# Performance work log

Measured on AMD Instinct MI355X. Metric: run time of the kernel, lower is better.

## Reference

```python
import jax, jax.numpy as jnp
import numpy as np
from math import comb

K = 10
N_NODES = 100000
NUM_FEATURES = 512
HIDDEN = 256
NUM_CLASSES = 64
N_EDGES = 3200000


def setup_inputs() -> dict:
    key = jax.random.key(0)
    k = jax.random.split(key, 8)
    x = jax.random.normal(k[0], (N_NODES, NUM_FEATURES), dtype=jnp.float32)
    src = jax.random.randint(k[1], (N_EDGES,), 0, N_NODES, dtype=jnp.int32)
    dst = jax.random.randint(k[2], (N_EDGES,), 0, N_NODES, dtype=jnp.int32)
    # symmetrize so the sym-normalized Laplacian is well-defined (undirected graph)
    src2 = jnp.concatenate([src, dst])
    dst2 = jnp.concatenate([dst, src])
    edge_index = jnp.stack([src2, dst2], axis=0)  # [2, 2E]
    s1 = 1.0 / np.sqrt(NUM_FEATURES)
    s2 = 1.0 / np.sqrt(HIDDEN)
    W1 = jax.random.uniform(k[3], (NUM_FEATURES, HIDDEN), jnp.float32, -s1, s1)
    b1 = jax.random.uniform(k[4], (HIDDEN,), jnp.float32, -s1, s1)
    W2 = jax.random.uniform(k[5], (HIDDEN, NUM_CLASSES), jnp.float32, -s2, s2)
    b2 = jax.random.uniform(k[6], (NUM_CLASSES,), jnp.float32, -s2, s2)
    temp = jnp.ones((K + 1,), dtype=jnp.float32)  # reset_parameters fills with 1
    return {"x": x, "edge_index": edge_index, "W1": W1, "b1": b1, "W2": W2, "b2": b2, "temp": temp}


def bern_prop(h, src, dst, temp, num_nodes):
    # sym-normalized adjacency weights: w = d^{-1/2}[src] * d^{-1/2}[dst]
    deg = jax.ops.segment_sum(jnp.ones_like(src, dtype=h.dtype), src, num_segments=num_nodes)
    dis = jnp.where(deg > 0, jax.lax.rsqrt(jnp.maximum(deg, 1e-30)), 0.0)
    w = dis[src] * dis[dst]  # [E]

    def adj(v):  # A_hat @ v via gather + scatter-add (source_to_target flow)
        return jax.ops.segment_sum(w[:, None] * v[src], dst, num_segments=num_nodes)

    TEMP = jax.nn.relu(temp)
    coef = np.array([comb(K, i) / 2.0 ** K for i in range(K + 1)], dtype=np.float32)

    tmp = [h]
    for _ in range(K):  # (2I - L) h = h + A_hat h
        h = h + adj(h)
        tmp.append(h)
    out = coef[0] * TEMP[0] * tmp[K]
    for i in range(K):
        y = tmp[K - i - 1]
        for _ in range(i + 1):  # L y = y - A_hat y
            y = y - adj(y)
        out = out + coef[i + 1] * TEMP[i + 1] * y
    return out


def reference(x, edge_index, W1, b1, W2, b2, temp):
    # eval mode: dropout is identity
    h = jax.nn.relu(x @ W1 + b1)
    h = h @ W2 + b2  # [N, num_classes]
    src, dst = edge_index[0], edge_index[1]
    h = bern_prop(h, src, dst, temp, x.shape[0])
    return jax.nn.log_softmax(h, axis=1)
```

## Files before the change

kernel.cpp:

```cpp
#include <hip/hip_runtime.h>
#include <hip/hip_bf16.h>
#include <hip/hip_cooperative_groups.h>
#include <math.h>


#define KORD 10

namespace cg = cooperative_groups;

typedef __attribute__((ext_vector_type(8))) short bf16x8;
typedef __attribute__((ext_vector_type(4))) float f32x4;

typedef __attribute__((address_space(1))) const unsigned int* gas_t;
typedef __attribute__((address_space(3))) unsigned int* las_t;

static __device__ __forceinline__ void gll16(const void* g, void* l) {
    __builtin_amdgcn_global_load_lds((gas_t)g, (las_t)l, 16, 0, 0);
}

static __device__ __forceinline__ ushort f2bf(float f) {
    unsigned u = __float_as_uint(f);
    unsigned r = (u + 0x7fffu + ((u >> 16) & 1u)) >> 16;
    return (ushort)r;
}
static __device__ __forceinline__ float bf2f(ushort h) {
    return __uint_as_float(((unsigned)h) << 16);
}
static __device__ __forceinline__ uint pack2(float a, float b) {
    return (uint)f2bf(a) | ((uint)f2bf(b) << 16);
}

__global__ void prep_all(const float* __restrict__ temp,
                         const float* __restrict__ W1, const float* __restrict__ W2,
                         float* __restrict__ acoef, int* __restrict__ flags,
                         ushort* __restrict__ w1b,
                         ushort* __restrict__ w2h, ushort* __restrict__ w2l)
{
    int tid = blockIdx.x * 256 + threadIdx.x;
    if (tid == 0) {
        int C[KORD + 1][KORD + 1];
        for (int n = 0; n <= KORD; ++n) {
            for (int k = 0; k <= KORD; ++k) C[n][k] = 0;
            C[n][0] = 1;
            for (int k = 1; k <= n; ++k)
                C[n][k] = C[n - 1][k - 1] + ((k <= n - 1) ? C[n - 1][k] : 0);
        }
        float a[KORD + 1];
        for (int j = 0; j <= KORD; ++j) a[j] = 0.f;
        for (int m = 0; m <= KORD; ++m) {
            float tm = temp[m];
            tm = tm > 0.f ? tm : 0.f;
            float cm = (float)C[KORD][m] / 1024.0f;
            for (int p = 0; p <= m; ++p)
                for (int q = 0; q <= KORD - m; ++q) {
                    int Mij = ((p & 1) ? -1 : 1) * C[m][p] * C[KORD - m][q];
                    a[p + q] += cm * tm * (float)Mij;
                }
        }
        for (int j = 0; j <= KORD; ++j) acoef[j] = a[j];
        int any = 0;
        for (int j = KORD; j >= 0; --j) {
            if (a[j] != 0.f) any = 1;
            flags[j] = any;
        }
    }
    if (tid < 512 * 256) {
        int j = tid & 7, lg = (tid >> 3) & 3, col = (tid >> 5) & 255, kt = tid >> 13;
        int k = kt * 32 + lg * 8 + j;
        w1b[tid] = f2bf(W1[k * 256 + col]);
    } else if (tid < 512 * 256 + 256 * 64) {
        int t2 = tid - 512 * 256;
        int j = t2 & 7, lg = (t2 >> 3) & 3, col = (t2 >> 5) & 63, ks = t2 >> 11;
        int k = ks * 32 + lg * 8 + j;
        float v = W2[k * 64 + col];
        ushort hi = f2bf(v);
        ushort lo = f2bf(v - bf2f(hi));
        w2h[t2] = hi; w2l[t2] = lo;
    }
}

__global__ __launch_bounds__(512, 4) void mlp_kernel(
    const float* __restrict__ x,
    const ushort* __restrict__ w1b,
    const ushort* __restrict__ w2h, const ushort* __restrict__ w2l,
    const float* __restrict__ b1, const float* __restrict__ b2,
    float* __restrict__ v0, float* __restrict__ out,
    const float* __restrict__ acoef, const int* __restrict__ flags, int N)
{
    __shared__ __align__(16) char sm[65536];

    const int t    = threadIdx.x;
    const int lane = t & 63;
    const int wid  = t >> 6;
    const int wm   = wid >> 2;
    const int wn   = wid & 3;
    const int l15  = lane & 15;
    const int lg   = lane >> 4;
    const int tile = blockIdx.x;
    const int row0 = tile * 128;

    f32x4 acc[4][4];
#pragma unroll
    for (int i = 0; i < 4; ++i)
#pragma unroll
        for (int j = 0; j < 4; ++j) acc[i][j] = (f32x4)0.f;

    const int sr = t >> 2;
    const int sq = t & 3;
    int rl = row0 + sr; if (rl > N - 1) rl = N - 1;
    const float* xsrc = x + (size_t)rl * 512 + sq * 8;
    ushort* xb0 = (ushort*)sm;
    ushort* xb1 = (ushort*)(sm + 8192);
    uint4* xdst0 = (uint4*)(sm + t * 16);
    uint4* xdst1 = (uint4*)(sm + 8192 + t * 16);

    const char* w1base = (const char*)w1b;
    char* bb0 = sm + 16384;
    char* bb1 = sm + 32768;

    float4 xa0 = *(const float4*)(xsrc);
    float4 xa1 = *(const float4*)(xsrc + 4);
#pragma unroll
    for (int i = 0; i < 2; ++i)
        gll16(w1base + (size_t)wid * 2048 + i * 1024 + lane * 16,
              bb0 + wid * 2048 + i * 1024);
    float4 xc0 = *(const float4*)(xsrc + 32);
    float4 xc1 = *(const float4*)(xsrc + 36);
    *xdst0 = make_uint4(pack2(xa0.x, xa0.y), pack2(xa0.z, xa0.w),
                        pack2(xa1.x, xa1.y), pack2(xa1.z, xa1.w));
    __syncthreads();

    for (int kt2 = 0; kt2 < 16; kt2 += 2) {
        {
            int ktn = kt2 + 1;
#pragma unroll
            for (int i = 0; i < 2; ++i)
                gll16(w1base + (size_t)ktn * 16384 + wid * 2048 + i * 1024 + lane * 16,
                      bb1 + wid * 2048 + i * 1024);
            int ktx = kt2 + 2; if (ktx > 15) ktx = 15;
            xa0 = *(const float4*)(xsrc + ktx * 32);
            xa1 = *(const float4*)(xsrc + ktx * 32 + 4);

            bf16x8 Ah[4];
#pragma unroll
            for (int mf = 0; mf < 4; ++mf)
                Ah[mf] = *(const bf16x8*)&xb0[((wm * 4 + mf) * 64 + l15 * 4 + lg) * 8];
#pragma unroll
            for (int nf = 0; nf < 4; ++nf) {
                bf16x8 B = *(const bf16x8*)(bb0 + (wn * 64 + nf * 16 + l15) * 64 + lg * 16);
#pragma unroll
                for (int mf = 0; mf < 4; ++mf)
                    acc[mf][nf] = __builtin_amdgcn_mfma_f32_16x16x32_bf16(Ah[mf], B, acc[mf][nf], 0, 0, 0);
            }
            *xdst1 = make_uint4(pack2(xc0.x, xc0.y), pack2(xc0.z, xc0.w),
                                pack2(xc1.x, xc1.y), pack2(xc1.z, xc1.w));
            __syncthreads();
        }
        {
            int ktn = kt2 + 2; if (ktn > 15) ktn = 15;
#pragma unroll
            for (int i = 0; i < 2; ++i)
                gll16(w1base + (size_t)ktn * 16384 + wid * 2048 + i * 1024 + lane * 16,
                      bb0 + wid * 2048 + i * 1024);
            int ktx = kt2 + 3; if (ktx > 15) ktx = 15;
            xc0 = *(const float4*)(xsrc + ktx * 32);
            xc1 = *(const float4*)(xsrc + ktx * 32 + 4);

            bf16x8 Ah[4];
#pragma unroll
            for (int mf = 0; mf < 4; ++mf)
                Ah[mf] = *(const bf16x8*)&xb1[((wm * 4 + mf) * 64 + l15 * 4 + lg) * 8];
#pragma unroll
            for (int nf = 0; nf < 4; ++nf) {
                bf16x8 B = *(const bf16x8*)(bb1 + (wn * 64 + nf * 16 + l15) * 64 + lg * 16);
#pragma unroll
                for (int mf = 0; mf < 4; ++mf)
                    acc[mf][nf] = __builtin_amdgcn_mfma_f32_16x16x32_bf16(Ah[mf], B, acc[mf][nf], 0, 0, 0);
            }
            *xdst0 = make_uint4(pack2(xa0.x, xa0.y), pack2(xa0.z, xa0.w),
                                pack2(xa1.x, xa1.y), pack2(xa1.z, xa1.w));
            __syncthreads();
        }
    }

    ushort* h1l = (ushort*)sm;
#pragma unroll
    for (int nf = 0; nf < 4; ++nf) {
        int col = wn * 64 + nf * 16 + l15;
        float bb = b1[col];
        int ks = col >> 5, lgw = (col >> 3) & 3, j = col & 7;
#pragma unroll
        for (int mf = 0; mf < 4; ++mf) {
            int g = wm * 4 + mf;
#pragma unroll
            for (int r = 0; r < 4; ++r) {
                float v = acc[mf][nf][r] + bb;
                v = fmaxf(v, 0.f);
                int l15w = lg * 4 + r;
                h1l[(((ks * 8 + g) * 64) + l15w * 4 + lgw) * 8 + j] = f2bf(v);
            }
        }
    }
    __syncthreads();

    f32x4 acc2[4];
#pragma unroll
    for (int i = 0; i < 4; ++i) acc2[i] = (f32x4)0.f;
#pragma unroll
    for (int ks = 0; ks < 8; ++ks) {
        bf16x8 A = *(const bf16x8*)&h1l[((ks * 8 + wid) * 64 + l15 * 4 + lg) * 8];
#pragma unroll
        for (int nf = 0; nf < 4; ++nf) {
            size_t bo = (size_t)ks * 2048 + (nf * 16 + l15) * 32 + (lg << 3);
            bf16x8 Bh = *(const bf16x8*)(w2h + bo);
            bf16x8 Bl = *(const bf16x8*)(w2l + bo);
            acc2[nf] = __builtin_amdgcn_mfma_f32_16x16x32_bf16(A, Bh, acc2[nf], 0, 0, 0);
            acc2[nf] = __builtin_amdgcn_mfma_f32_16x16x32_bf16(A, Bl, acc2[nf], 0, 0, 0);
        }
    }

    int flag1 = flags[0 + 1];
    float a0c = acoef[0];
    float z[4][4];
#pragma unroll
    for (int nf = 0; nf < 4; ++nf) {
        float bb = b2[nf * 16 + l15];
#pragma unroll
        for (int r = 0; r < 4; ++r) z[nf][r] = acc2[nf][r] + bb;
    }
    if (!flag1) {
#pragma unroll
        for (int r = 0; r < 4; ++r) {
            int row = row0 + wid * 16 + lg * 4 + r;
            float mx = fmaxf(fmaxf(z[0][r], z[1][r]), fmaxf(z[2][r], z[3][r]));
#pragma unroll
            for (int off = 1; off < 16; off <<= 1) mx = fmaxf(mx, __shfl_xor(mx, off, 64));
            float s = expf(z[0][r] - mx) + expf(z[1][r] - mx)
                    + expf(z[2][r] - mx) + expf(z[3][r] - mx);
#pragma unroll
            for (int off = 1; off < 16; off <<= 1) s += __shfl_xor(s, off, 64);
            float lns = logf(s);
            if (row < N) {
#pragma unroll
                for (int nf = 0; nf < 4; ++nf)
                    out[(size_t)row * 64 + nf * 16 + l15] = z[nf][r] - mx - lns;
            }
        }
    } else {
#pragma unroll
        for (int nf = 0; nf < 4; ++nf) {
            int col = nf * 16 + l15;
#pragma unroll
            for (int r = 0; r < 4; ++r) {
                int row = row0 + wid * 16 + lg * 4 + r;
                if (row < N) {
                    size_t o = (size_t)row * 64 + col;
                    v0[o] = z[nf][r];
                    out[o] = a0c * z[nf][r];
                }
            }
        }
    }
}

__global__ __launch_bounds__(256) void graph_coop(
    const int* __restrict__ src, const int* __restrict__ dst, int E, int N,
    int* __restrict__ degs, int* __restrict__ degd, int* __restrict__ cursor,
    int* __restrict__ rowp, int* __restrict__ csrs, float* __restrict__ csrw,
    float* __restrict__ v0, float* __restrict__ v1, float* __restrict__ out,
    const float* __restrict__ acoef, const int* __restrict__ flags)
{
    __shared__ int sums[256];
    if (!flags[1]) return;
    cg::grid_group grid = cg::this_grid();
    int gtid = blockIdx.x * 256 + threadIdx.x;
    int gstr = gridDim.x * 256;

    for (int i = gtid; i < N; i += gstr) { degs[i] = 0; degd[i] = 0; cursor[i] = 0; }
    grid.sync();
    for (int e = gtid; e < E; e += gstr) {
        atomicAdd(&degs[src[e]], 1);
        atomicAdd(&degd[dst[e]], 1);
    }
    grid.sync();
    if (blockIdx.x == 0) {
        int tid = threadIdx.x;
        int chunk = (N + 255) / 256;
        int s0 = tid * chunk;
        int s1 = s0 + chunk; if (s1 > N) s1 = N; if (s0 > N) s0 = N;
        int s = 0;
        for (int i = s0; i < s1; ++i) s += degd[i];
        sums[tid] = s;
        __syncthreads();
        for (int off = 1; off < 256; off <<= 1) {
            int v = (tid >= off) ? sums[tid - off] : 0;
            __syncthreads();
            sums[tid] += v;
            __syncthreads();
        }
        int run = sums[tid] - s;
        for (int i = s0; i < s1; ++i) { rowp[i] = run; run += degd[i]; }
        if (tid == 255) rowp[N] = sums[255];
    }
    grid.sync();
    for (int e = gtid; e < E; e += gstr) {
        int s = src[e], d = dst[e];
        int dgs = degs[s], dgd = degs[d];
        float ws_ = (dgs > 0 ? rsqrtf((float)dgs) : 0.f)
                  * (dgd > 0 ? rsqrtf((float)dgd) : 0.f);
        int slot = rowp[d] + atomicAdd(&cursor[d], 1);
        csrs[slot] = s;
        csrw[slot] = ws_;
    }
    grid.sync();
    const float* va = v0;
    float* vb = v1;
    int lane = threadIdx.x & 63;
    int grpbase = lane & 48;
    for (int j = 1; j <= KORD; ++j) {
        if (!flags[j]) break;
        float aj = acoef[j];
        for (int idx = gtid; idx < N * 16; idx += gstr) {
            int n = idx >> 4;
            int q = idx & 15;
            int beg = rowp[n], end = rowp[n + 1];
            float4 acc = make_float4(0.f, 0.f, 0.f, 0.f);
            for (int base = beg; base < end; base += 16) {
                int s = 0; float wvv = 0.f;
                int ii = base + q;
                if (ii < end) { s = csrs[ii]; wvv = csrw[ii]; }
                int m = end - base; if (m > 16) m = 16;
                for (int u = 0; u < m; ++u) {
                    int ss = __shfl(s, grpbase + u, 64);
                    float ww = __shfl(wvv, grpbase + u, 64);
                    float4 vv = *(const float4*)(va + ((long)ss << 6) + (q << 2));
                    acc.x += ww * vv.x; acc.y += ww * vv.y;
                    acc.z += ww * vv.z; acc.w += ww * vv.w;
                }
            }
            long o = ((long)n << 6) + (q << 2);
            *(float4*)(vb + o) = acc;
            float4 ov = *(const float4*)(out + o);
            ov.x += aj * acc.x; ov.y += aj * acc.y;
            ov.z += aj * acc.z; ov.w += aj * acc.w;
            *(float4*)(out + o) = ov;
        }
        grid.sync();
        float* tsw = vb; vb = (float*)va; va = tsw;
    }
    for (int idx = gtid; idx < N * 64; idx += gstr) {
        int n = idx >> 6;
        int c = idx & 63;
        float v = out[(long)n * 64 + c];
        float mx = v;
#pragma unroll
        for (int off = 32; off; off >>= 1) mx = fmaxf(mx, __shfl_xor(mx, off, 64));
        float e = expf(v - mx);
        float s = e;
#pragma unroll
        for (int off = 32; off; off >>= 1) s += __shfl_xor(s, off, 64);
        out[(long)n * 64 + c] = v - mx - logf(s);
    }
}

extern "C" void kernel_launch(void* const* d_in, const int* in_sizes, int n_in,
                              void* d_out, int out_size, void* d_ws, size_t ws_size,
                              hipStream_t stream)
{
    const float* x    = (const float*)d_in[0];
    const int*   ei   = (const int*)d_in[1];
    const float* W1   = (const float*)d_in[2];
    const float* b1   = (const float*)d_in[3];
    const float* W2   = (const float*)d_in[4];
    const float* b2   = (const float*)d_in[5];
    const float* temp = (const float*)d_in[6];

    int N = in_sizes[0] / 512;
    int E = in_sizes[1] / 2;
    const int* src = ei;
    const int* dst = ei + E;
    float* out = (float*)d_out;

    char* w = (char*)d_ws;
    auto alloc = [&](size_t bytes) {
        char* p = w;
        w += (bytes + 255) & ~(size_t)255;
        return p;
    };
    float* acoef  = (float*)alloc(64);
    int*   flags  = (int*)alloc(64);
    int*   degs   = (int*)alloc((size_t)N * 4);
    int*   degd   = (int*)alloc((size_t)N * 4);
    int*   cursor = (int*)alloc((size_t)N * 4);
    int*   rowp   = (int*)alloc((size_t)(N + 1) * 4);
    int*   csrs   = (int*)alloc((size_t)E * 4);
    float* csrw   = (float*)alloc((size_t)E * 4);
    ushort* w1b   = (ushort*)alloc(512 * 256 * 2);
    ushort* w2h   = (ushort*)alloc(256 * 64 * 2);
    ushort* w2l   = (ushort*)alloc(256 * 64 * 2);
    float* v0     = (float*)alloc((size_t)N * 64 * 4);
    float* v1     = (float*)alloc((size_t)N * 64 * 4);

    prep_all<<<576, 256, 0, stream>>>(temp, W1, W2, acoef, flags, w1b, w2h, w2l);

    int ntiles = (N + 127) / 128;
    mlp_kernel<<<ntiles, 512, 0, stream>>>(x, w1b, w2h, w2l, b1, b2, v0, out,
                                           acoef, flags, N);

    int Ei = E, Ni = N;
    void* cargs[] = {
        (void*)&src, (void*)&dst, (void*)&Ei, (void*)&Ni,
        (void*)&degs, (void*)&degd, (void*)&cursor, (void*)&rowp,
        (void*)&csrs, (void*)&csrw, (void*)&v0, (void*)&v1, (void*)&out,
        (void*)&acoef, (void*)&flags
    };
    hipLaunchCooperativeKernel((void*)graph_coop, dim3(1024), dim3(256),
                               cargs, 0, stream);
}
```

Baseline: 101.1 us.

## Drop LDS staging in MLP GEMM, load operands directly from global

Rewrites the first GEMM so each wave loads its x rows and W1 fragments straight from global memory into registers, with no LDS double buffering or block barriers in the K loop. Tiles shrink from 128 to 64 rows per block, and each wave now computes 16 rows by 128 columns. The goal is to remove barrier stalls and LDS traffic and to let more blocks fit per CU. In exchange, W1 is re-read from global or L2 by every wave, and half the waves sit idle during the second GEMM and epilogue.

```diff
diff --git a/kernel.cpp b/kernel.cpp
--- a/kernel.cpp
+++ b/kernel.cpp
@@ -11,13 +11,6 @@
 typedef __attribute__((ext_vector_type(8))) short bf16x8;
 typedef __attribute__((ext_vector_type(4))) float f32x4;
 
-typedef __attribute__((address_space(1))) const unsigned int* gas_t;
-typedef __attribute__((address_space(3))) unsigned int* las_t;
-
-static __device__ __forceinline__ void gll16(const void* g, void* l) {
-    __builtin_amdgcn_global_load_lds((gas_t)g, (las_t)l, 16, 0, 0);
-}
-
 static __device__ __forceinline__ ushort f2bf(float f) {
     unsigned u = __float_as_uint(f);
     unsigned r = (u + 0x7fffu + ((u >> 16) & 1u)) >> 16;
@@ -28,6 +21,11 @@
 }
 static __device__ __forceinline__ uint pack2(float a, float b) {
     return (uint)f2bf(a) | ((uint)f2bf(b) << 16);
+}
+static __device__ __forceinline__ bf16x8 mk8(uint a, uint b, uint c, uint d) {
+    union { uint4 u; bf16x8 v; } x;
+    x.u = make_uint4(a, b, c, d);
+    return x.v;
 }
 
 __global__ void prep_all(const float* __restrict__ temp,
@@ -87,128 +85,66 @@
     float* __restrict__ v0, float* __restrict__ out,
     const float* __restrict__ acoef, const int* __restrict__ flags, int N)
 {
-    __shared__ __align__(16) char sm[65536];
+    __shared__ __align__(16) ushort h1l[64 * 256];
 
     const int t    = threadIdx.x;
     const int lane = t & 63;
     const int wid  = t >> 6;
-    const int wm   = wid >> 2;
-    const int wn   = wid & 3;
+    const int wm   = wid >> 1;
+    const int wn   = wid & 1;
     const int l15  = lane & 15;
     const int lg   = lane >> 4;
-    const int tile = blockIdx.x;
-    const int row0 = tile * 128;
-
-    f32x4 acc[4][4];
-#pragma unroll
-    for (int i = 0; i < 4; ++i)
-#pragma unroll
-        for (int j = 0; j < 4; ++j) acc[i][j] = (f32x4)0.f;
-
-    const int sr = t >> 2;
-    const int sq = t & 3;
-    int rl = row0 + sr; if (rl > N - 1) rl = N - 1;
-    const float* xsrc = x + (size_t)rl * 512 + sq * 8;
-    ushort* xb0 = (ushort*)sm;
-    ushort* xb1 = (ushort*)(sm + 8192);
-    uint4* xdst0 = (uint4*)(sm + t * 16);
-    uint4* xdst1 = (uint4*)(sm + 8192 + t * 16);
-
-    const char* w1base = (const char*)w1b;
-    char* bb0 = sm + 16384;
-    char* bb1 = sm + 32768;
-
-    float4 xa0 = *(const float4*)(xsrc);
-    float4 xa1 = *(const float4*)(xsrc + 4);
-#pragma unroll
-    for (int i = 0; i < 2; ++i)
-        gll16(w1base + (size_t)wid * 2048 + i * 1024 + lane * 16,
-              bb0 + wid * 2048 + i * 1024);
-    float4 xc0 = *(const float4*)(xsrc + 32);
-    float4 xc1 = *(const float4*)(xsrc + 36);
-    *xdst0 = make_uint4(pack2(xa0.x, xa0.y), pack2(xa0.z, xa0.w),
-                        pack2(xa1.x, xa1.y), pack2(xa1.z, xa1.w));
-    __syncthreads();
-
-    for (int kt2 = 0; kt2 < 16; kt2 += 2) {
-        {
-            int ktn = kt2 + 1;
-#pragma unroll
-            for (int i = 0; i < 2; ++i)
-                gll16(w1base + (size_t)ktn * 16384 + wid * 2048 + i * 1024 + lane * 16,
-                      bb1 + wid * 2048 + i * 1024);
-            int ktx = kt2 + 2; if (ktx > 15) ktx = 15;
-            xa0 = *(const float4*)(xsrc + ktx * 32);
-            xa1 = *(const float4*)(xsrc + ktx * 32 + 4);
-
-            bf16x8 Ah[4];
-#pragma unroll
-            for (int mf = 0; mf < 4; ++mf)
-                Ah[mf] = *(const bf16x8*)&xb0[((wm * 4 + mf) * 64 + l15 * 4 + lg) * 8];
-#pragma unroll
-            for (int nf = 0; nf < 4; ++nf) {
-                bf16x8 B = *(const bf16x8*)(bb0 + (wn * 64 + nf * 16 + l15) * 64 + lg * 16);
-#pragma unroll
-                for (int mf = 0; mf < 4; ++mf)
-                    acc[mf][nf] = __builtin_amdgcn_mfma_f32_16x16x32_bf16(Ah[mf], B, acc[mf][nf], 0, 0, 0);
-            }
-            *xdst1 = make_uint4(pack2(xc0.x, xc0.y), pack2(xc0.z, xc0.w),
-                                pack2(xc1.x, xc1.y), pack2(xc1.z, xc1.w));
-            __syncthreads();
-        }
-        {
-            int ktn = kt2 + 2; if (ktn > 15) ktn = 15;
-#pragma unroll
-            for (int i = 0; i < 2; ++i)
-                gll16(w1base + (size_t)ktn * 16384 + wid * 2048 + i * 1024 + lane * 16,
-                      bb0 + wid * 2048 + i * 1024);
-            int ktx = kt2 + 3; if (ktx > 15) ktx = 15;
-            xc0 = *(const float4*)(xsrc + ktx * 32);
-            xc1 = *(const float4*)(xsrc + ktx * 32 + 4);
-
-            bf16x8 Ah[4];
-#pragma unroll
-            for (int mf = 0; mf < 4; ++mf)
-                Ah[mf] = *(const bf16x8*)&xb1[((wm * 4 + mf) * 64 + l15 * 4 + lg) * 8];
-#pragma unroll
-            for (int nf = 0; nf < 4; ++nf) {
-                bf16x8 B = *(const bf16x8*)(bb1 + (wn * 64 + nf * 16 + l15) * 64 + lg * 16);
-#pragma unroll
-                for (int mf = 0; mf < 4; ++mf)
-                    acc[mf][nf] = __builtin_amdgcn_mfma_f32_16x16x32_bf16(Ah[mf], B, acc[mf][nf], 0, 0, 0);
-            }
-            *xdst0 = make_uint4(pack2(xa0.x, xa0.y), pack2(xa0.z, xa0.w),
-                                pack2(xa1.x, xa1.y), pack2(xa1.z, xa1.w));
-            __syncthreads();
-        }
-    }
-
-    ushort* h1l = (ushort*)sm;
-#pragma unroll
-    for (int nf = 0; nf < 4; ++nf) {
-        int col = wn * 64 + nf * 16 + l15;
+    const int row0 = blockIdx.x * 64;
+
+    int grow = row0 + wm * 16 + l15;
+    if (grow > N - 1) grow = N - 1;
+    const float* xp = x + (size_t)grow * 512 + lg * 8;
+    const ushort* bp = w1b + (wn * 128 + l15) * 32 + lg * 8;
+
+    f32x4 acc[8];
+#pragma unroll
+    for (int i = 0; i < 8; ++i) acc[i] = (f32x4)0.f;
+
+    float4 a0 = *(const float4*)(xp);
+    float4 a1 = *(const float4*)(xp + 4);
+#pragma unroll 2
+    for (int kt = 0; kt < 16; ++kt) {
+        int ktx = kt + 1; if (ktx > 15) ktx = 15;
+        float4 n0 = *(const float4*)(xp + ktx * 32);
+        float4 n1 = *(const float4*)(xp + ktx * 32 + 4);
+        bf16x8 A = mk8(pack2(a0.x, a0.y), pack2(a0.z, a0.w),
+                       pack2(a1.x, a1.y), pack2(a1.z, a1.w));
+        const ushort* bkt = bp + kt * 8192;
+#pragma unroll
+        for (int nf = 0; nf < 8; ++nf) {
+            bf16x8 B = *(const bf16x8*)(bkt + nf * 512);
+            acc[nf] = __builtin_amdgcn_mfma_f32_16x16x32_bf16(A, B, acc[nf], 0, 0, 0);
+        }
+        a0 = n0; a1 = n1;
+    }
+
+#pragma unroll
+    for (int nf = 0; nf < 8; ++nf) {
+        int col = wn * 128 + nf * 16 + l15;
         float bb = b1[col];
         int ks = col >> 5, lgw = (col >> 3) & 3, j = col & 7;
 #pragma unroll
-        for (int mf = 0; mf < 4; ++mf) {
-            int g = wm * 4 + mf;
-#pragma unroll
-            for (int r = 0; r < 4; ++r) {
-                float v = acc[mf][nf][r] + bb;
-                v = fmaxf(v, 0.f);
-                int l15w = lg * 4 + r;
-                h1l[(((ks * 8 + g) * 64) + l15w * 4 + lgw) * 8 + j] = f2bf(v);
-            }
+        for (int r = 0; r < 4; ++r) {
+            float v = fmaxf(acc[nf][r] + bb, 0.f);
+            int lrow = lg * 4 + r;
+            h1l[((ks * 4 + wm) * 64 + lrow * 4 + lgw) * 8 + j] = f2bf(v);
         }
     }
     __syncthreads();
 
+    if (wid >= 4) return;
+
     f32x4 acc2[4];
 #pragma unroll
     for (int i = 0; i < 4; ++i) acc2[i] = (f32x4)0.f;
 #pragma unroll
     for (int ks = 0; ks < 8; ++ks) {
-        bf16x8 A = *(const bf16x8*)&h1l[((ks * 8 + wid) * 64 + l15 * 4 + lg) * 8];
+        bf16x8 A = *(const bf16x8*)&h1l[((ks * 4 + wid) * 64 + l15 * 4 + lg) * 8];
 #pragma unroll
         for (int nf = 0; nf < 4; ++nf) {
             size_t bo = (size_t)ks * 2048 + (nf * 16 + l15) * 32 + (lg << 3);
@@ -219,7 +155,7 @@
         }
     }
 
-    int flag1 = flags[0 + 1];
+    int flag1 = flags[1];
     float a0c = acoef[0];
     float z[4][4];
 #pragma unroll
@@ -403,7 +339,7 @@
 
     prep_all<<<576, 256, 0, stream>>>(temp, W1, W2, acoef, flags, w1b, w2h, w2l);
 
-    int ntiles = (N + 127) / 128;
+    int ntiles = (N + 63) / 64;
     mlp_kernel<<<ntiles, 512, 0, stream>>>(x, w1b, w2h, w2l, b1, b2, v0, out,
                                            acoef, flags, N);
 
```

After: 212.3 us. 2.1x slower.
